# Kernel optimization log

Measured on AMD Instinct MI355X. Metric: run time of the kernel, lower is better.

Reference implementation:

```python
import jax, jax.numpy as jnp
import numpy as np

HEADS = 16
NEG = -1e9  # matches masked_fill(-1000000000.0)

def setup_inputs() -> dict:
    key = jax.random.key(0)
    ks = jax.random.split(key, 7)
    B, T, C = 2, 2048, 1024
    s = 1.0 / np.sqrt(C)
    return {
        "q": jax.random.normal(ks[0], (B, T, C), jnp.float32),
        "k": jax.random.normal(ks[1], (B, T, C), jnp.float32),
        "v": jax.random.normal(ks[2], (B, T, C), jnp.float32),
        "Wq": jax.random.normal(ks[3], (C, C), jnp.float32) * s,
        "Wk": jax.random.normal(ks[4], (C, C), jnp.float32) * s,
        "Wv": jax.random.normal(ks[5], (C, C), jnp.float32) * s,
        "Wo": jax.random.normal(ks[6], (C, C), jnp.float32) * s,
    }

def reference(q, k, v, Wq, Wk, Wv, Wo):
    B, T, C = q.shape
    h = HEADS
    dk = C // h
    # torch Linear (no bias): y = x @ W.T ; weight is [out, in]
    def proj(x, W):
        return (x @ W.T).reshape(B, T, h, dk).transpose(0, 2, 1, 3)  # [B,h,T,dk]
    qh, kh, vh = proj(q, Wq), proj(k, Wk), proj(v, Wv)
    scale = jnp.asarray(dk, q.dtype) ** 0.5
    scores = jnp.einsum('bhqd,bhkd->bhqk', qh / scale, kh)  # [B,h,T,T]
    causal = jnp.tril(jnp.ones((T, T), dtype=bool))
    scores = jnp.where(causal[None, None], scores, jnp.asarray(NEG, scores.dtype))
    attn = jax.nn.softmax(scores, axis=-1)
    out = jnp.einsum('bhqk,bhkd->bhqd', attn, vh)  # [B,h,T,dk]
    concat = out.transpose(0, 2, 1, 3).reshape(B, T, C)
    return concat @ Wo.T
```

## Files before the change

kernel.cpp:

```cpp
#include <hip/hip_runtime.h>
#include <hip/hip_bf16.h>

typedef __bf16 bf16x8 __attribute__((ext_vector_type(8)));
typedef float  f32x4  __attribute__((ext_vector_type(4)));
typedef unsigned short u16;

__device__ __forceinline__ u16 f2bf(float f) {
    __bf16 h = (__bf16)f;
    return __builtin_bit_cast(u16, h);
}

__device__ __forceinline__ f32x4 mfma16(bf16x8 a, bf16x8 b, f32x4 c) {
    return __builtin_amdgcn_mfma_f32_16x16x32_bf16(a, b, c, 0, 0, 0);
}

__global__ __launch_bounds__(256) void cvt4(const float* __restrict__ W0,
                                            const float* __restrict__ W1,
                                            const float* __restrict__ W2,
                                            const float* __restrict__ W3,
                                            u16* __restrict__ dst) {
    const int t     = blockIdx.x * 256 + threadIdx.x;
    const int which = t >> 17;
    const int off   = (t & 0x1FFFF) * 8;
    const float* s  = (which == 0) ? W0 : (which == 1) ? W1 : (which == 2) ? W2 : W3;
    float4 f0 = *(const float4*)(s + off);
    float4 f1 = *(const float4*)(s + off + 4);
    bf16x8 u;
    u[0] = (__bf16)f0.x; u[1] = (__bf16)f0.y; u[2] = (__bf16)f0.z; u[3] = (__bf16)f0.w;
    u[4] = (__bf16)f1.x; u[5] = (__bf16)f1.y; u[6] = (__bf16)f1.z; u[7] = (__bf16)f1.w;
    *(bf16x8*)(dst + ((size_t)which << 20) + off) = u;
}

__global__ __launch_bounds__(256) void gemm_qkv(const float* __restrict__ q,
                                                const float* __restrict__ k,
                                                const float* __restrict__ v,
                                                const u16* __restrict__ Wb,
                                                u16* __restrict__ Qp,
                                                u16* __restrict__ Kp,
                                                u16* __restrict__ Vt) {
    constexpr int K = 1024, N = 1024;
    __shared__ u16 As[128 * 32];
    __shared__ u16 Bs[128 * 32];

    const int tid  = threadIdx.x;
    const int lane = tid & 63;
    const int w    = tid >> 6;
    const int wr = w >> 1, wc = w & 1;
    const int wg    = (blockIdx.x & 7) * 96 + (blockIdx.x >> 3);
    const int which = wg >> 8;
    const int inner = wg & 255;
    const int m0 = (inner >> 3) * 128, n0 = (inner & 7) * 128;
    const int colg = lane & 15, rowg = lane >> 4;

    const float* A = (which == 0) ? q : (which == 1) ? k : v;
    const u16*   W = Wb + ((size_t)which << 20);

    f32x4 acc[4][4];
#pragma unroll
    for (int i = 0; i < 4; ++i)
#pragma unroll
        for (int j = 0; j < 4; ++j) acc[i][j] = (f32x4){0.f, 0.f, 0.f, 0.f};

    for (int kk = 0; kk < K; kk += 32) {
#pragma unroll
        for (int i = 0; i < 2; ++i) {
            const int c   = i * 256 + tid;
            const int row = c >> 2;
            const int cg  = (c & 3) * 8;
            {
                const float* g = A + (size_t)(m0 + row) * K + kk + cg;
                float4 f0 = *(const float4*)g;
                float4 f1 = *(const float4*)(g + 4);
                bf16x8 u;
                u[0] = (__bf16)f0.x; u[1] = (__bf16)f0.y; u[2] = (__bf16)f0.z; u[3] = (__bf16)f0.w;
                u[4] = (__bf16)f1.x; u[5] = (__bf16)f1.y; u[6] = (__bf16)f1.z; u[7] = (__bf16)f1.w;
                *(bf16x8*)(&As[c * 8]) = u;
            }
            {
                const u16* g = W + (size_t)(n0 + row) * K + kk + cg;
                *(uint4*)(&Bs[c * 8]) = *(const uint4*)g;
            }
        }
        __syncthreads();

        bf16x8 af[4], bfr[4];
#pragma unroll
        for (int mi = 0; mi < 4; ++mi)
            af[mi] = *(const bf16x8*)(&As[(wr * 64 + mi * 16 + colg) * 32 + rowg * 8]);
#pragma unroll
        for (int ni = 0; ni < 4; ++ni)
            bfr[ni] = *(const bf16x8*)(&Bs[(wc * 64 + ni * 16 + colg) * 32 + rowg * 8]);
#pragma unroll
        for (int mi = 0; mi < 4; ++mi)
#pragma unroll
            for (int ni = 0; ni < 4; ++ni)
                acc[mi][ni] = mfma16(af[mi], bfr[ni], acc[mi][ni]);
        __syncthreads();
    }

    u16* Crm = (which == 0) ? Qp : Kp;
#pragma unroll
    for (int mi = 0; mi < 4; ++mi) {
#pragma unroll
        for (int ni = 0; ni < 4; ++ni) {
#pragma unroll
            for (int r = 0; r < 4; ++r) {
                const int row = m0 + wr * 64 + mi * 16 + rowg * 4 + r;
                const int col = n0 + wc * 64 + ni * 16 + colg;
                const float vv = acc[mi][ni][r];
                if (which < 2) {
                    Crm[(size_t)row * N + col] = f2bf(vv);
                } else {
                    const int b = row >> 11, t = row & 2047;
                    const int h = col >> 6,  d = col & 63;
                    Vt[((size_t)((b * 16 + h) * 64 + d) << 11) + t] = f2bf(vv);
                }
            }
        }
    }
}

__global__ __launch_bounds__(256) void gemm_out(const u16* __restrict__ Ap,
                                                const u16* __restrict__ W,
                                                float* __restrict__ Cp) {
    constexpr int K = 1024, N = 1024;
    __shared__ u16 As[64 * 32];
    __shared__ u16 Bs[128 * 32];

    const int tid  = threadIdx.x;
    const int lane = tid & 63;
    const int w    = tid >> 6;
    const int wr = w >> 1, wc = w & 1;
    const int wg = (blockIdx.x & 7) * 64 + (blockIdx.x >> 3);
    const int m0 = (wg >> 3) * 64, n0 = (wg & 7) * 128;
    const int colg = lane & 15, rowg = lane >> 4;

    f32x4 acc[2][4];
#pragma unroll
    for (int i = 0; i < 2; ++i)
#pragma unroll
        for (int j = 0; j < 4; ++j) acc[i][j] = (f32x4){0.f, 0.f, 0.f, 0.f};

    for (int kk = 0; kk < K; kk += 32) {
        {
            const int c   = tid;
            const int row = c >> 2;
            const int cg  = (c & 3) * 8;
            const u16* g  = Ap + (size_t)(m0 + row) * K + kk + cg;
            *(uint4*)(&As[c * 8]) = *(const uint4*)g;
        }
#pragma unroll
        for (int i = 0; i < 2; ++i) {
            const int c   = i * 256 + tid;
            const int row = c >> 2;
            const int cg  = (c & 3) * 8;
            const u16* g  = W + (size_t)(n0 + row) * K + kk + cg;
            *(uint4*)(&Bs[c * 8]) = *(const uint4*)g;
        }
        __syncthreads();

        bf16x8 af[2], bfr[4];
#pragma unroll
        for (int mi = 0; mi < 2; ++mi)
            af[mi] = *(const bf16x8*)(&As[(wr * 32 + mi * 16 + colg) * 32 + rowg * 8]);
#pragma unroll
        for (int ni = 0; ni < 4; ++ni)
            bfr[ni] = *(const bf16x8*)(&Bs[(wc * 64 + ni * 16 + colg) * 32 + rowg * 8]);
#pragma unroll
        for (int mi = 0; mi < 2; ++mi)
#pragma unroll
            for (int ni = 0; ni < 4; ++ni)
                acc[mi][ni] = mfma16(af[mi], bfr[ni], acc[mi][ni]);
        __syncthreads();
    }

#pragma unroll
    for (int mi = 0; mi < 2; ++mi)
#pragma unroll
        for (int ni = 0; ni < 4; ++ni)
#pragma unroll
            for (int r = 0; r < 4; ++r) {
                const int row = m0 + wr * 32 + mi * 16 + rowg * 4 + r;
                const int col = n0 + wc * 64 + ni * 16 + colg;
                Cp[(size_t)row * N + col] = acc[mi][ni][r];
            }
}

constexpr float CEXP = 0.18033688011112042f;

__global__ __launch_bounds__(256) void attn_causal(const u16* __restrict__ Qp,
                                                   const u16* __restrict__ Kp,
                                                   const u16* __restrict__ Vt,
                                                   u16* __restrict__ concat) {
    constexpr int T = 2048, C = 1024;
    __shared__ __align__(16) u16 Ks[128 * 64];
    __shared__ __align__(16) u16 Vs[64 * 128];
    __shared__ __align__(16) u16 Pl[4][2048];

    const int tid  = threadIdx.x;
    const int lane = tid & 63;
    const int w    = tid >> 6;
    const int colg = lane & 15, rowg = lane >> 4;

    const int idx = blockIdx.x;
    const int xcd = idx & 7;
    const int i1  = idx >> 3;
    const int bh  = xcd * 4 + (i1 & 3);
    const int qg  = 31 - (i1 >> 2);
    const int b = bh >> 4, h = bh & 15;

    const int q0 = (qg * 4 + w) * 16;
    const int nt    = (q0 + 143) >> 7;
    const int ktmax = ((qg * 4 + 3) * 16 + 143) >> 7;

    const char* Kg = (const char*)(Kp + (size_t)(b * T) * C + h * 64);
    const char* Vg = (const char*)(Vt + ((size_t)(b * 16 + h) * 64) * T);
    char* Ksb = (char*)Ks;
    char* Vsb = (char*)Vs;
    char* Pw  = (char*)&Pl[w][0];

    const u16* Qb = Qp + (size_t)(b * T + q0 + colg) * C + h * 64;
    const bf16x8 qf0 = *(const bf16x8*)(Qb + rowg * 8);
    const bf16x8 qf1 = *(const bf16x8*)(Qb + 32 + rowg * 8);

    float mm = -1e30f, ll = 0.f;
    f32x4 O[4];
#pragma unroll
    for (int g = 0; g < 4; ++g) O[g] = (f32x4){0.f, 0.f, 0.f, 0.f};

    const int sw = (colg & 7) << 4;

    for (int kt = 0; kt < ktmax; ++kt) {
        const int kvb = kt * 128;
        uint4 kst[4], vst[4];
#pragma unroll
        for (int i2 = 0; i2 < 4; ++i2) {
            const int s  = i2 * 4096 + tid * 16;
            const int kv = s >> 7, ir = s & 127;
            kst[i2] = *(const uint4*)(Kg + (size_t)(kvb + kv) * 2048 + ir);
            const int d = s >> 8, irv = s & 255;
            vst[i2] = *(const uint4*)(Vg + (size_t)d * 4096 + (size_t)kvb * 2 + irv);
        }
#pragma unroll
        for (int i2 = 0; i2 < 4; ++i2) {
            const int s  = i2 * 4096 + tid * 16;
            const int kv = s >> 7;
            *(uint4*)(Ksb + (s ^ ((kv & 7) << 4))) = kst[i2];
            const int d = s >> 8;
            *(uint4*)(Vsb + (s ^ ((d & 7) << 4))) = vst[i2];
        }
        __syncthreads();

        if (kt < nt) {
            float pr[8][4];
#pragma unroll
            for (int sub = 0; sub < 8; ++sub) {
                const int kb = (sub * 16 + colg) * 128 + rowg * 16;
                bf16x8 kf0 = *(const bf16x8*)(Ksb + (kb ^ sw));
                bf16x8 kf1 = *(const bf16x8*)(Ksb + ((kb + 64) ^ sw));
                f32x4 t = (f32x4){0.f, 0.f, 0.f, 0.f};
                t = mfma16(kf0, qf0, t);
                t = mfma16(kf1, qf1, t);
#pragma unroll
                for (int r = 0; r < 4; ++r) pr[sub][r] = t[r];
            }
            if (kvb + 127 > q0) {
#pragma unroll
                for (int sub = 0; sub < 8; ++sub)
#pragma unroll
                    for (int r = 0; r < 4; ++r)
                        if (kvb + sub * 16 + rowg * 4 + r > q0 + colg) pr[sub][r] = -1e30f;
            }
            float mx[8];
#pragma unroll
            for (int sub = 0; sub < 8; ++sub)
                mx[sub] = fmaxf(fmaxf(pr[sub][0], pr[sub][1]), fmaxf(pr[sub][2], pr[sub][3]));
            float pm = fmaxf(fmaxf(fmaxf(mx[0], mx[1]), fmaxf(mx[2], mx[3])),
                             fmaxf(fmaxf(mx[4], mx[5]), fmaxf(mx[6], mx[7])));
            pm = fmaxf(pm, __shfl_xor(pm, 16, 64));
            pm = fmaxf(pm, __shfl_xor(pm, 32, 64));
            if (__any(pm > mm + 40.f)) {
                const float mn = fmaxf(mm, pm);
                const float sc = __builtin_amdgcn_exp2f((mm - mn) * CEXP);
                mm = mn;
                ll *= sc;
#pragma unroll
                for (int r = 0; r < 4; ++r) {
                    const float scr = __shfl(sc, (lane & 48) + rowg * 4 + r, 64);
#pragma unroll
                    for (int g = 0; g < 4; ++g) O[g][r] *= scr;
                }
            }
            float rs = 0.f;
#pragma unroll
            for (int sub = 0; sub < 8; ++sub) {
                const float e0 = __builtin_amdgcn_exp2f((pr[sub][0] - mm) * CEXP);
                const float e1 = __builtin_amdgcn_exp2f((pr[sub][1] - mm) * CEXP);
                const float e2 = __builtin_amdgcn_exp2f((pr[sub][2] - mm) * CEXP);
                const float e3 = __builtin_amdgcn_exp2f((pr[sub][3] - mm) * CEXP);
                pr[sub][0] = e0; pr[sub][1] = e1; pr[sub][2] = e2; pr[sub][3] = e3;
                rs += (e0 + e1) + (e2 + e3);
            }
            rs += __shfl_xor(rs, 16, 64);
            rs += __shfl_xor(rs, 32, 64);
            ll += rs;
#pragma unroll
            for (int sub = 0; sub < 8; ++sub) {
                uint2 pk;
                pk.x = (unsigned)f2bf(pr[sub][0]) | ((unsigned)f2bf(pr[sub][1]) << 16);
                pk.y = (unsigned)f2bf(pr[sub][2]) | ((unsigned)f2bf(pr[sub][3]) << 16);
                const int wb = (colg * 256 + sub * 32 + rowg * 8) ^ sw;
                *(uint2*)(Pw + wb) = pk;
            }
            bf16x8 pf[4];
#pragma unroll
            for (int kc = 0; kc < 4; ++kc)
                pf[kc] = *(const bf16x8*)(Pw + ((colg * 256 + kc * 64 + rowg * 16) ^ sw));
#pragma unroll
            for (int g = 0; g < 4; ++g) {
                const int vb0 = (g * 16 + colg) * 256 + rowg * 16;
#pragma unroll
                for (int kc = 0; kc < 4; ++kc) {
                    bf16x8 vf = *(const bf16x8*)(Vsb + ((vb0 + kc * 64) ^ sw));
                    O[g] = mfma16(pf[kc], vf, O[g]);
                }
            }
        }
        __syncthreads();
    }

#pragma unroll
    for (int r = 0; r < 4; ++r) {
        const float lr = __shfl(ll, (lane & 48) + rowg * 4 + r, 64);
        const float rc = 1.f / lr;
        const size_t base = (size_t)(b * T + q0 + rowg * 4 + r) * C + h * 64;
#pragma unroll
        for (int g = 0; g < 4; ++g)
            concat[base + g * 16 + colg] = f2bf(O[g][r] * rc);
    }
}

extern "C" void kernel_launch(void* const* d_in, const int* in_sizes, int n_in,
                              void* d_out, int out_size, void* d_ws, size_t ws_size,
                              hipStream_t stream) {
    const float* q  = (const float*)d_in[0];
    const float* k  = (const float*)d_in[1];
    const float* v  = (const float*)d_in[2];
    const float* Wq = (const float*)d_in[3];
    const float* Wk = (const float*)d_in[4];
    const float* Wv = (const float*)d_in[5];
    const float* Wo = (const float*)d_in[6];
    float* out = (float*)d_out;

    constexpr size_t NELEM = (size_t)4096 * 1024;
    constexpr size_t WSZ   = (size_t)1 << 20;
    u16* Wb = (u16*)d_ws;
    u16* Qp = Wb + 4 * WSZ;
    u16* Kp = Qp + NELEM;
    u16* Vt = Kp + NELEM;
    u16* Cc = Vt + NELEM;

    cvt4<<<2048, 256, 0, stream>>>(Wq, Wk, Wv, Wo, Wb);

    gemm_qkv<<<768, 256, 0, stream>>>(q, k, v, Wb, Qp, Kp, Vt);

    attn_causal<<<1024, 256, 0, stream>>>(Qp, Kp, Vt, Cc);

    gemm_out<<<512, 256, 0, stream>>>(Cc, Wb + 3 * WSZ, out);
}
```

Before: 137.2 us.

## Double-buffer projection GEMMs with direct global-to-LDS loads and fragment-ordered layout

Both projection GEMMs now prefetch the next K-slice while the current one is computed. Weight (and, in the output GEMM, activation) tiles are copied straight into LDS with global_load_lds into double buffers, and the fp32 inputs of the QKV GEMM are held in registers one step ahead. The shared-memory tiles are stored in MFMA fragment order so each lane reads one contiguous 16-byte chunk, and the output GEMM drops one barrier per iteration. The goal is to hide global-load latency and cut LDS bank conflicts, at the cost of more LDS and registers and tighter synchronisation correctness.

```diff
diff --git a/kernel.cpp b/kernel.cpp
--- a/kernel.cpp
+++ b/kernel.cpp
@@ -12,6 +12,12 @@
 
 __device__ __forceinline__ f32x4 mfma16(bf16x8 a, bf16x8 b, f32x4 c) {
     return __builtin_amdgcn_mfma_f32_16x16x32_bf16(a, b, c, 0, 0, 0);
+}
+
+__device__ __forceinline__ void gload16(const u16* g, u16* l) {
+    __builtin_amdgcn_global_load_lds(
+        (const __attribute__((address_space(1))) void*)g,
+        (__attribute__((address_space(3))) void*)l, 16, 0, 0);
 }
 
 __global__ __launch_bounds__(256) void cvt4(const float* __restrict__ W0,
@@ -39,8 +45,8 @@
                                                 u16* __restrict__ Kp,
                                                 u16* __restrict__ Vt) {
     constexpr int K = 1024, N = 1024;
-    __shared__ u16 As[128 * 32];
-    __shared__ u16 Bs[128 * 32];
+    __shared__ __align__(16) u16 As[4096];
+    __shared__ __align__(16) u16 Bs[2][4096];
 
     const int tid  = threadIdx.x;
     const int lane = tid & 63;
@@ -55,41 +61,67 @@
     const float* A = (which == 0) ? q : (which == 1) ? k : v;
     const u16*   W = Wb + ((size_t)which << 20);
 
+    const float* PA[2];
+    int dA[2];
+    const u16* PB[2];
+    int dB[2];
+#pragma unroll
+    for (int i = 0; i < 2; ++i) {
+        const int c    = i * 256 + tid;
+        const int rowA = c >> 2;
+        const int kcA  = c & 3;
+        PA[i] = A + (size_t)(m0 + rowA) * K + kcA * 8;
+        dA[i] = (rowA >> 6) * 2048 + ((rowA >> 4) & 3) * 512 + (kcA * 16 + (rowA & 15)) * 8;
+        const int rowB = (c >> 8) * 64 + ((c >> 6) & 3) * 16 + (c & 15);
+        const int k8B  = ((c >> 4) & 3) * 8;
+        PB[i] = W + (size_t)(n0 + rowB) * K + k8B;
+        dB[i] = c * 8;
+    }
+
     f32x4 acc[4][4];
 #pragma unroll
     for (int i = 0; i < 4; ++i)
 #pragma unroll
         for (int j = 0; j < 4; ++j) acc[i][j] = (f32x4){0.f, 0.f, 0.f, 0.f};
 
-    for (int kk = 0; kk < K; kk += 32) {
+    float4 a0[2], a1[2];
+#pragma unroll
+    for (int i = 0; i < 2; ++i) {
+        a0[i] = *(const float4*)(PA[i]);
+        a1[i] = *(const float4*)(PA[i] + 4);
+        gload16(PB[i], &Bs[0][dB[i]]);
+    }
+
+    for (int t = 0; t < 32; ++t) {
 #pragma unroll
         for (int i = 0; i < 2; ++i) {
-            const int c   = i * 256 + tid;
-            const int row = c >> 2;
-            const int cg  = (c & 3) * 8;
-            {
-                const float* g = A + (size_t)(m0 + row) * K + kk + cg;
-                float4 f0 = *(const float4*)g;
-                float4 f1 = *(const float4*)(g + 4);
-                bf16x8 u;
-                u[0] = (__bf16)f0.x; u[1] = (__bf16)f0.y; u[2] = (__bf16)f0.z; u[3] = (__bf16)f0.w;
-                u[4] = (__bf16)f1.x; u[5] = (__bf16)f1.y; u[6] = (__bf16)f1.z; u[7] = (__bf16)f1.w;
-                *(bf16x8*)(&As[c * 8]) = u;
-            }
-            {
-                const u16* g = W + (size_t)(n0 + row) * K + kk + cg;
-                *(uint4*)(&Bs[c * 8]) = *(const uint4*)g;
-            }
+            bf16x8 u;
+            u[0] = (__bf16)a0[i].x; u[1] = (__bf16)a0[i].y;
+            u[2] = (__bf16)a0[i].z; u[3] = (__bf16)a0[i].w;
+            u[4] = (__bf16)a1[i].x; u[5] = (__bf16)a1[i].y;
+            u[6] = (__bf16)a1[i].z; u[7] = (__bf16)a1[i].w;
+            *(bf16x8*)(&As[dA[i]]) = u;
         }
         __syncthreads();
 
+        if (t < 31) {
+            const int kk = (t + 1) * 32;
+#pragma unroll
+            for (int i = 0; i < 2; ++i) {
+                gload16(PB[i] + kk, &Bs[(t + 1) & 1][dB[i]]);
+                a0[i] = *(const float4*)(PA[i] + kk);
+                a1[i] = *(const float4*)(PA[i] + kk + 4);
+            }
+        }
+
+        const u16* Bcur = &Bs[t & 1][0];
         bf16x8 af[4], bfr[4];
 #pragma unroll
         for (int mi = 0; mi < 4; ++mi)
-            af[mi] = *(const bf16x8*)(&As[(wr * 64 + mi * 16 + colg) * 32 + rowg * 8]);
+            af[mi] = *(const bf16x8*)(&As[wr * 2048 + mi * 512 + lane * 8]);
 #pragma unroll
         for (int ni = 0; ni < 4; ++ni)
-            bfr[ni] = *(const bf16x8*)(&Bs[(wc * 64 + ni * 16 + colg) * 32 + rowg * 8]);
+            bfr[ni] = *(const bf16x8*)(Bcur + wc * 2048 + ni * 512 + lane * 8);
 #pragma unroll
         for (int mi = 0; mi < 4; ++mi)
 #pragma unroll
@@ -124,8 +156,8 @@
                                                 const u16* __restrict__ W,
                                                 float* __restrict__ Cp) {
     constexpr int K = 1024, N = 1024;
-    __shared__ u16 As[64 * 32];
-    __shared__ u16 Bs[128 * 32];
+    __shared__ __align__(16) u16 Ao[2][2048];
+    __shared__ __align__(16) u16 Bo[2][4096];
 
     const int tid  = threadIdx.x;
     const int lane = tid & 63;
@@ -135,43 +167,56 @@
     const int m0 = (wg >> 3) * 64, n0 = (wg & 7) * 128;
     const int colg = lane & 15, rowg = lane >> 4;
 
+    const int cA   = tid;
+    const int rowA = (cA >> 7) * 32 + ((cA >> 6) & 1) * 16 + (cA & 15);
+    const int k8A  = ((cA >> 4) & 3) * 8;
+    const u16* PAo = Ap + (size_t)(m0 + rowA) * K + k8A;
+    const int dAo  = cA * 8;
+
+    const u16* PB[2];
+    int dB[2];
+#pragma unroll
+    for (int i = 0; i < 2; ++i) {
+        const int c    = i * 256 + tid;
+        const int rowB = (c >> 8) * 64 + ((c >> 6) & 3) * 16 + (c & 15);
+        const int k8B  = ((c >> 4) & 3) * 8;
+        PB[i] = W + (size_t)(n0 + rowB) * K + k8B;
+        dB[i] = c * 8;
+    }
+
     f32x4 acc[2][4];
 #pragma unroll
     for (int i = 0; i < 2; ++i)
 #pragma unroll
         for (int j = 0; j < 4; ++j) acc[i][j] = (f32x4){0.f, 0.f, 0.f, 0.f};
 
-    for (int kk = 0; kk < K; kk += 32) {
-        {
-            const int c   = tid;
-            const int row = c >> 2;
-            const int cg  = (c & 3) * 8;
-            const u16* g  = Ap + (size_t)(m0 + row) * K + kk + cg;
-            *(uint4*)(&As[c * 8]) = *(const uint4*)g;
-        }
-#pragma unroll
-        for (int i = 0; i < 2; ++i) {
-            const int c   = i * 256 + tid;
-            const int row = c >> 2;
-            const int cg  = (c & 3) * 8;
-            const u16* g  = W + (size_t)(n0 + row) * K + kk + cg;
-            *(uint4*)(&Bs[c * 8]) = *(const uint4*)g;
-        }
+    gload16(PAo, &Ao[0][dAo]);
+#pragma unroll
+    for (int i = 0; i < 2; ++i) gload16(PB[i], &Bo[0][dB[i]]);
+
+    for (int t = 0; t < 32; ++t) {
         __syncthreads();
-
+        if (t < 31) {
+            const int kk = (t + 1) * 32;
+            gload16(PAo + kk, &Ao[(t + 1) & 1][dAo]);
+#pragma unroll
+            for (int i = 0; i < 2; ++i)
+                gload16(PB[i] + kk, &Bo[(t + 1) & 1][dB[i]]);
+        }
+        const u16* Acur = &Ao[t & 1][0];
+        const u16* Bcur = &Bo[t & 1][0];
         bf16x8 af[2], bfr[4];
 #pragma unroll
         for (int mi = 0; mi < 2; ++mi)
-            af[mi] = *(const bf16x8*)(&As[(wr * 32 + mi * 16 + colg) * 32 + rowg * 8]);
+            af[mi] = *(const bf16x8*)(Acur + wr * 1024 + mi * 512 + lane * 8);
 #pragma unroll
         for (int ni = 0; ni < 4; ++ni)
-            bfr[ni] = *(const bf16x8*)(&Bs[(wc * 64 + ni * 16 + colg) * 32 + rowg * 8]);
+            bfr[ni] = *(const bf16x8*)(Bcur + wc * 2048 + ni * 512 + lane * 8);
 #pragma unroll
         for (int mi = 0; mi < 2; ++mi)
 #pragma unroll
             for (int ni = 0; ni < 4; ++ni)
                 acc[mi][ni] = mfma16(af[mi], bfr[ni], acc[mi][ni]);
-        __syncthreads();
     }
 
 #pragma unroll
```

After: 151.8 us. +10.7%, slower.

## Pre-convert activations to bf16 and use direct global-to-LDS loads in GEMMs

Applied to the files above, without the earlier changes.

Moves the fp32-to-bf16 conversion of q/k/v into the upfront conversion kernel alongside the weights, so both projection GEMMs load pure bf16 tiles. The GEMMs now use global_load_lds (direct buffer-to-LDS) with a pre-swizzled fragment-major LDS layout and a K-step of 64. The output GEMM is enlarged to 128x128 tiles. Costs an extra bf16 write and read of the activations through the workspace, and uses more LDS per block, which may lower occupancy.

```diff
diff --git a/kernel.cpp b/kernel.cpp
--- a/kernel.cpp
+++ b/kernel.cpp
@@ -14,33 +14,51 @@
     return __builtin_amdgcn_mfma_f32_16x16x32_bf16(a, b, c, 0, 0, 0);
 }
 
-__global__ __launch_bounds__(256) void cvt4(const float* __restrict__ W0,
-                                            const float* __restrict__ W1,
-                                            const float* __restrict__ W2,
-                                            const float* __restrict__ W3,
+__device__ __forceinline__ void gload16(const u16* g, u16* l) {
+    __builtin_amdgcn_global_load_lds(
+        (const __attribute__((address_space(1))) void*)g,
+        (__attribute__((address_space(3))) void*)l, 16, 0, 0);
+}
+
+__global__ __launch_bounds__(256) void cvt7(const float* __restrict__ q,
+                                            const float* __restrict__ k,
+                                            const float* __restrict__ v,
+                                            const float* __restrict__ Wq,
+                                            const float* __restrict__ Wk,
+                                            const float* __restrict__ Wv,
+                                            const float* __restrict__ Wo,
                                             u16* __restrict__ dst) {
-    const int t     = blockIdx.x * 256 + threadIdx.x;
-    const int which = t >> 17;
-    const int off   = (t & 0x1FFFF) * 8;
-    const float* s  = (which == 0) ? W0 : (which == 1) ? W1 : (which == 2) ? W2 : W3;
+    const int t = blockIdx.x * 256 + threadIdx.x;
+    const float* s;
+    int o;
+    if (t < 0x80000)       { s = q; o = t; }
+    else if (t < 0x100000) { s = k; o = t - 0x80000; }
+    else if (t < 0x180000) { s = v; o = t - 0x100000; }
+    else {
+        const int r = t - 0x180000;
+        const int w = r >> 17;
+        o = r & 0x1FFFF;
+        s = (w == 0) ? Wq : (w == 1) ? Wk : (w == 2) ? Wv : Wo;
+    }
+    const int off = o * 8;
     float4 f0 = *(const float4*)(s + off);
     float4 f1 = *(const float4*)(s + off + 4);
     bf16x8 u;
     u[0] = (__bf16)f0.x; u[1] = (__bf16)f0.y; u[2] = (__bf16)f0.z; u[3] = (__bf16)f0.w;
     u[4] = (__bf16)f1.x; u[5] = (__bf16)f1.y; u[6] = (__bf16)f1.z; u[7] = (__bf16)f1.w;
-    *(bf16x8*)(dst + ((size_t)which << 20) + off) = u;
-}
-
-__global__ __launch_bounds__(256) void gemm_qkv(const float* __restrict__ q,
-                                                const float* __restrict__ k,
-                                                const float* __restrict__ v,
+    *(bf16x8*)(dst + (size_t)t * 8) = u;
+}
+
+__global__ __launch_bounds__(256) void gemm_qkv(const u16* __restrict__ qb,
+                                                const u16* __restrict__ kb,
+                                                const u16* __restrict__ vb,
                                                 const u16* __restrict__ Wb,
                                                 u16* __restrict__ Qp,
                                                 u16* __restrict__ Kp,
                                                 u16* __restrict__ Vt) {
     constexpr int K = 1024, N = 1024;
-    __shared__ u16 As[128 * 32];
-    __shared__ u16 Bs[128 * 32];
+    __shared__ __align__(16) u16 As[8192];
+    __shared__ __align__(16) u16 Bs[8192];
 
     const int tid  = threadIdx.x;
     const int lane = tid & 63;
@@ -52,8 +70,20 @@
     const int m0 = (inner >> 3) * 128, n0 = (inner & 7) * 128;
     const int colg = lane & 15, rowg = lane >> 4;
 
-    const float* A = (which == 0) ? q : (which == 1) ? k : v;
-    const u16*   W = Wb + ((size_t)which << 20);
+    const u16* A = (which == 0) ? qb : (which == 1) ? kb : vb;
+    const u16* W = Wb + ((size_t)which << 20);
+
+    size_t soff[4];
+    int dofs[4];
+#pragma unroll
+    for (int i = 0; i < 4; ++i) {
+        const int c = i * 256 + tid;
+        const int g = c >> 6, l = c & 63;
+        const int row = (g & 7) * 16 + (l & 15);
+        const int kof = (g >> 3) * 32 + (l >> 4) * 8;
+        soff[i] = (size_t)row * K + kof;
+        dofs[i] = c * 8;
+    }
 
     f32x4 acc[4][4];
 #pragma unroll
@@ -61,40 +91,33 @@
 #pragma unroll
         for (int j = 0; j < 4; ++j) acc[i][j] = (f32x4){0.f, 0.f, 0.f, 0.f};
 
-    for (int kk = 0; kk < K; kk += 32) {
-#pragma unroll
-        for (int i = 0; i < 2; ++i) {
-            const int c   = i * 256 + tid;
-            const int row = c >> 2;
-            const int cg  = (c & 3) * 8;
-            {
-                const float* g = A + (size_t)(m0 + row) * K + kk + cg;
-                float4 f0 = *(const float4*)g;
-                float4 f1 = *(const float4*)(g + 4);
-                bf16x8 u;
-                u[0] = (__bf16)f0.x; u[1] = (__bf16)f0.y; u[2] = (__bf16)f0.z; u[3] = (__bf16)f0.w;
-                u[4] = (__bf16)f1.x; u[5] = (__bf16)f1.y; u[6] = (__bf16)f1.z; u[7] = (__bf16)f1.w;
-                *(bf16x8*)(&As[c * 8]) = u;
-            }
-            {
-                const u16* g = W + (size_t)(n0 + row) * K + kk + cg;
-                *(uint4*)(&Bs[c * 8]) = *(const uint4*)g;
-            }
-        }
-        __syncthreads();
-
-        bf16x8 af[4], bfr[4];
-#pragma unroll
-        for (int mi = 0; mi < 4; ++mi)
-            af[mi] = *(const bf16x8*)(&As[(wr * 64 + mi * 16 + colg) * 32 + rowg * 8]);
-#pragma unroll
-        for (int ni = 0; ni < 4; ++ni)
-            bfr[ni] = *(const bf16x8*)(&Bs[(wc * 64 + ni * 16 + colg) * 32 + rowg * 8]);
-#pragma unroll
-        for (int mi = 0; mi < 4; ++mi)
+    const u16* Abase = A + (size_t)m0 * K;
+    const u16* Bbase = W + (size_t)n0 * K;
+
+    for (int t = 0; t < 16; ++t) {
+        const int kk = t * 64;
+#pragma unroll
+        for (int i = 0; i < 4; ++i) {
+            gload16(Abase + soff[i] + kk, &As[dofs[i]]);
+            gload16(Bbase + soff[i] + kk, &Bs[dofs[i]]);
+        }
+        __syncthreads();
+
+#pragma unroll
+        for (int ks = 0; ks < 2; ++ks) {
+            bf16x8 af[4], bfr[4];
+#pragma unroll
+            for (int mi = 0; mi < 4; ++mi)
+                af[mi] = *(const bf16x8*)(&As[(ks * 8 + wr * 4 + mi) * 512 + lane * 8]);
 #pragma unroll
             for (int ni = 0; ni < 4; ++ni)
-                acc[mi][ni] = mfma16(af[mi], bfr[ni], acc[mi][ni]);
+                bfr[ni] = *(const bf16x8*)(&Bs[(ks * 8 + wc * 4 + ni) * 512 + lane * 8]);
+#pragma unroll
+            for (int mi = 0; mi < 4; ++mi)
+#pragma unroll
+                for (int ni = 0; ni < 4; ++ni)
+                    acc[mi][ni] = mfma16(af[mi], bfr[ni], acc[mi][ni]);
+        }
         __syncthreads();
     }
 
@@ -111,9 +134,9 @@
                 if (which < 2) {
                     Crm[(size_t)row * N + col] = f2bf(vv);
                 } else {
-                    const int b = row >> 11, t = row & 2047;
+                    const int b = row >> 11, tt = row & 2047;
                     const int h = col >> 6,  d = col & 63;
-                    Vt[((size_t)((b * 16 + h) * 64 + d) << 11) + t] = f2bf(vv);
+                    Vt[((size_t)((b * 16 + h) * 64 + d) << 11) + tt] = f2bf(vv);
                 }
             }
         }
@@ -124,63 +147,72 @@
                                                 const u16* __restrict__ W,
                                                 float* __restrict__ Cp) {
     constexpr int K = 1024, N = 1024;
-    __shared__ u16 As[64 * 32];
-    __shared__ u16 Bs[128 * 32];
+    __shared__ __align__(16) u16 As[8192];
+    __shared__ __align__(16) u16 Bs[8192];
 
     const int tid  = threadIdx.x;
     const int lane = tid & 63;
     const int w    = tid >> 6;
     const int wr = w >> 1, wc = w & 1;
-    const int wg = (blockIdx.x & 7) * 64 + (blockIdx.x >> 3);
-    const int m0 = (wg >> 3) * 64, n0 = (wg & 7) * 128;
+    const int wg = (blockIdx.x & 7) * 32 + (blockIdx.x >> 3);
+    const int m0 = (wg >> 3) * 128, n0 = (wg & 7) * 128;
     const int colg = lane & 15, rowg = lane >> 4;
 
-    f32x4 acc[2][4];
-#pragma unroll
-    for (int i = 0; i < 2; ++i)
+    size_t soff[4];
+    int dofs[4];
+#pragma unroll
+    for (int i = 0; i < 4; ++i) {
+        const int c = i * 256 + tid;
+        const int g = c >> 6, l = c & 63;
+        const int row = (g & 7) * 16 + (l & 15);
+        const int kof = (g >> 3) * 32 + (l >> 4) * 8;
+        soff[i] = (size_t)row * K + kof;
+        dofs[i] = c * 8;
+    }
+
+    f32x4 acc[4][4];
+#pragma unroll
+    for (int i = 0; i < 4; ++i)
 #pragma unroll
         for (int j = 0; j < 4; ++j) acc[i][j] = (f32x4){0.f, 0.f, 0.f, 0.f};
 
-    for (int kk = 0; kk < K; kk += 32) {
-        {
-            const int c   = tid;
-            const int row = c >> 2;
-            const int cg  = (c & 3) * 8;
-            const u16* g  = Ap + (size_t)(m0 + row) * K + kk + cg;
-            *(uint4*)(&As[c * 8]) = *(const uint4*)g;
-        }
-#pragma unroll
-        for (int i = 0; i < 2; ++i) {
-            const int c   = i * 256 + tid;
-            const int row = c >> 2;
-            const int cg  = (c & 3) * 8;
-            const u16* g  = W + (size_t)(n0 + row) * K + kk + cg;
-            *(uint4*)(&Bs[c * 8]) = *(const uint4*)g;
-        }
-        __syncthreads();
-
-        bf16x8 af[2], bfr[4];
-#pragma unroll
-        for (int mi = 0; mi < 2; ++mi)
-            af[mi] = *(const bf16x8*)(&As[(wr * 32 + mi * 16 + colg) * 32 + rowg * 8]);
+    const u16* Abase = Ap + (size_t)m0 * K;
+    const u16* Bbase = W + (size_t)n0 * K;
+
+    for (int t = 0; t < 16; ++t) {
+        const int kk = t * 64;
+#pragma unroll
+        for (int i = 0; i < 4; ++i) {
+            gload16(Abase + soff[i] + kk, &As[dofs[i]]);
+            gload16(Bbase + soff[i] + kk, &Bs[dofs[i]]);
+        }
+        __syncthreads();
+
+#pragma unroll
+        for (int ks = 0; ks < 2; ++ks) {
+            bf16x8 af[4], bfr[4];
+#pragma unroll
+            for (int mi = 0; mi < 4; ++mi)
+                af[mi] = *(const bf16x8*)(&As[(ks * 8 + wr * 4 + mi) * 512 + lane * 8]);
+#pragma unroll
+            for (int ni = 0; ni < 4; ++ni)
+                bfr[ni] = *(const bf16x8*)(&Bs[(ks * 8 + wc * 4 + ni) * 512 + lane * 8]);
+#pragma unroll
+            for (int mi = 0; mi < 4; ++mi)
+#pragma unroll
+                for (int ni = 0; ni < 4; ++ni)
+                    acc[mi][ni] = mfma16(af[mi], bfr[ni], acc[mi][ni]);
+        }
+        __syncthreads();
+    }
+
+#pragma unroll
+    for (int mi = 0; mi < 4; ++mi)
 #pragma unroll
         for (int ni = 0; ni < 4; ++ni)
-            bfr[ni] = *(const bf16x8*)(&Bs[(wc * 64 + ni * 16 + colg) * 32 + rowg * 8]);
-#pragma unroll
-        for (int mi = 0; mi < 2; ++mi)
-#pragma unroll
-            for (int ni = 0; ni < 4; ++ni)
-                acc[mi][ni] = mfma16(af[mi], bfr[ni], acc[mi][ni]);
-        __syncthreads();
-    }
-
-#pragma unroll
-    for (int mi = 0; mi < 2; ++mi)
-#pragma unroll
-        for (int ni = 0; ni < 4; ++ni)
 #pragma unroll
             for (int r = 0; r < 4; ++r) {
-                const int row = m0 + wr * 32 + mi * 16 + rowg * 4 + r;
+                const int row = m0 + wr * 64 + mi * 16 + rowg * 4 + r;
                 const int col = n0 + wc * 64 + ni * 16 + colg;
                 Cp[(size_t)row * N + col] = acc[mi][ni][r];
             }
@@ -354,17 +386,20 @@
 
     constexpr size_t NELEM = (size_t)4096 * 1024;
     constexpr size_t WSZ   = (size_t)1 << 20;
-    u16* Wb = (u16*)d_ws;
-    u16* Qp = Wb + 4 * WSZ;
-    u16* Kp = Qp + NELEM;
-    u16* Vt = Kp + NELEM;
-    u16* Cc = Vt + NELEM;
-
-    cvt4<<<2048, 256, 0, stream>>>(Wq, Wk, Wv, Wo, Wb);
-
-    gemm_qkv<<<768, 256, 0, stream>>>(q, k, v, Wb, Qp, Kp, Vt);
+    u16* QB  = (u16*)d_ws;
+    u16* KB  = QB + NELEM;
+    u16* VB  = KB + NELEM;
+    u16* Wbf = VB + NELEM;
+    u16* Qp  = Wbf + 4 * WSZ;
+    u16* Kp  = Qp + NELEM;
+    u16* Vt  = Kp + NELEM;
+    u16* Cc  = Vt + NELEM;
+
+    cvt7<<<8192, 256, 0, stream>>>(q, k, v, Wq, Wk, Wv, Wo, QB);
+
+    gemm_qkv<<<768, 256, 0, stream>>>(QB, KB, VB, Wbf, Qp, Kp, Vt);
 
     attn_causal<<<1024, 256, 0, stream>>>(Qp, Kp, Vt, Cc);
 
-    gemm_out<<<512, 256, 0, stream>>>(Cc, Wb + 3 * WSZ, out);
-}
+    gemm_out<<<256, 256, 0, stream>>>(Cc, Wbf + 3 * WSZ, out);
+}
```

Result: slower. 176.6 us (+28.8%).
